# Optimization experiments

Hardware: AMD Instinct MI355X
Metric: run time of the kernel (lower is better)

## Reference

```python
import jax, jax.numpy as jnp
import numpy as np

T_STEPS = 200
B = 512
D = 32
LMBD = 1.0


def _socm_const_m_loss(ts, states, noises, controls, nabla_V, nabla_f,
                       nabla_b, nabla_g, sigma, log_pd, log_ps, log_tw):
    # ts: [T+1]; states/nabla_V: [T+1,B,D]; noises/controls/nabla_f: [T,B,D];
    # nabla_b: [T,B,D,D]; nabla_g: [B,D]; sigma: [D,D]; logs: [B]
    sigma_inv_T = jnp.linalg.inv(sigma).T

    # integrand terms on the first T timesteps ([:-1] slice in torch source)
    term1 = nabla_f  # nabla_f(ts[0], states)[:-1]
    sig_noises = jnp.einsum('ij,abj->abi', sigma_inv_T, noises)
    term2 = -np.sqrt(LMBD) * jnp.einsum('abij,abj->abi', nabla_b, sig_noises)
    sig_controls = jnp.einsum('ij,abj->abi', sigma_inv_T, controls)
    term3 = -jnp.einsum('abij,abj->abi', nabla_b, sig_controls)

    dts = ts[1:] - ts[:-1]                      # [T]
    dts_ = dts[:, None, None]
    zeros = jnp.zeros_like(term1[:1])           # [1,B,D]

    t1_dt = jnp.concatenate([zeros, term1 * dts_], axis=0)             # [T+1,B,D]
    t2_sdt = jnp.concatenate([zeros, term2 * jnp.sqrt(dts_)], axis=0)
    t3_dt = jnp.concatenate([zeros, term3 * dts_], axis=0)

    def rev_cum(x):
        # total_sum - cumsum == reverse cumulative sum starting at each step
        return jnp.sum(x, axis=0, keepdims=True) - jnp.cumsum(x, axis=0)

    least_squares_target = (rev_cum(t1_dt) + rev_cum(t2_sdt) + rev_cum(t3_dt)
                            + nabla_g[None, :, :])                     # [T+1,B,D]

    control_learned = -jnp.einsum('ij,tbj->tbi', sigma.T, nabla_V)
    control_target = -jnp.einsum('ij,tbj->tbi', sigma.T, least_squares_target)

    weight = jnp.exp(log_pd + log_ps + log_tw)  # [B]
    sq = (control_learned - control_target) ** 2 * weight[None, :, None]
    n_t, n_b = states.shape[0], states.shape[1]
    return jnp.sum(sq) / (n_t * n_b)


def setup_inputs() -> dict:
    key = jax.random.key(0)
    ks = jax.random.split(key, 11)
    ts = jnp.linspace(0.0, 1.0, T_STEPS + 1, dtype=jnp.float32)
    states = jax.random.normal(ks[0], (T_STEPS + 1, B, D), jnp.float32)
    noises = jax.random.normal(ks[1], (T_STEPS, B, D), jnp.float32)
    controls = jax.random.normal(ks[2], (T_STEPS, B, D), jnp.float32)
    nabla_V = jax.random.normal(ks[3], (T_STEPS + 1, B, D), jnp.float32)
    nabla_f = jax.random.normal(ks[4], (T_STEPS, B, D), jnp.float32)
    nabla_b = 0.1 * jax.random.normal(ks[5], (T_STEPS, B, D, D), jnp.float32)
    nabla_g = jax.random.normal(ks[6], (B, D), jnp.float32)
    sigma = jnp.eye(D, dtype=jnp.float32) + 0.05 * jax.random.normal(ks[7], (D, D), jnp.float32)
    log_pd = 0.01 * jax.random.normal(ks[8], (B,), jnp.float32)
    log_ps = 0.01 * jax.random.normal(ks[9], (B,), jnp.float32)
    log_tw = 0.01 * jax.random.normal(ks[10], (B,), jnp.float32)
    return {"ts": ts, "states": states, "noises": noises, "controls": controls,
            "nabla_V": nabla_V, "nabla_f": nabla_f, "nabla_b": nabla_b,
            "nabla_g": nabla_g, "sigma": sigma, "log_pd": log_pd,
            "log_ps": log_ps, "log_tw": log_tw}


def reference(ts, states, noises, controls, nabla_V, nabla_f, nabla_b,
              nabla_g, sigma, log_pd, log_ps, log_tw):
    return _socm_const_m_loss(ts, states, noises, controls, nabla_V, nabla_f,
                              nabla_b, nabla_g, sigma, log_pd, log_ps, log_tw)
```

## Files before the change

### kernel.cpp

```cpp
#include <hip/hip_runtime.h>
#include <math.h>

#define T_STEPS 200
#define BB 512
#define DD 32
#define LMBD 1.0f
#define NCH 4
#define CHT 50

#define WS_MINV 0
#define WS_A    1024
#define WS_W    2048
#define WS_PART 2560
#define WS_CT   3072
#define WS_Y    (3072 + 65536)
#define WS_M    (3072 + 131072)

__global__ __launch_bounds__(512) void prep_kernel(
    const float* __restrict__ sigma,
    const float* __restrict__ lpd, const float* __restrict__ lps,
    const float* __restrict__ ltw,
    float* __restrict__ ws)
{
    __shared__ float sg[32][33];
    const int tid = threadIdx.x;

    ws[WS_W + tid] = expf(lpd[tid] + lps[tid] + ltw[tid]);

    for (int idx = tid; idx < 1024; idx += 512)
        sg[idx >> 5][idx & 31] = sigma[idx];
    __syncthreads();

    for (int idx = tid; idx < 1024; idx += 512) {
        int i = idx >> 5, j = idx & 31;
        float s = 0.0f;
        #pragma unroll
        for (int k = 0; k < 32; ++k) s += sg[i][k] * sg[j][k];
        ws[WS_A + idx] = s;
    }

    if (tid < 64) {
        const int l = tid;
        float col[32];
        #pragma unroll
        for (int r = 0; r < 32; ++r) {
            float v = sg[r][l & 31];
            col[r] = (l < 32) ? v : ((r == (l - 32)) ? 1.0f : 0.0f);
        }
        #pragma unroll
        for (int k = 0; k < 32; ++k) {
            float pinv = 1.0f / __shfl(col[k], k);
            col[k] *= pinv;
            #pragma unroll
            for (int r = 0; r < 32; ++r) {
                if (r == k) continue;
                float f = __shfl(col[r], k);
                col[r] -= f * col[k];
            }
        }
        if (l >= 32) {
            #pragma unroll
            for (int r = 0; r < 32; ++r)
                ws[WS_MINV + (l - 32) * 32 + r] = col[r];
        }
    }
}

__global__ __launch_bounds__(256) void stream_kernel(
    const float* __restrict__ ts,
    const float* __restrict__ noises,
    const float* __restrict__ controls,
    const float* __restrict__ nabla_f,
    const float* __restrict__ nabla_V,
    const float* __restrict__ nabla_b,
    float* __restrict__ ws)
{
    __shared__ float ts_l[52];
    __shared__ __align__(16) float buf[2][4][32];
    __shared__ __align__(16) float vls[32];
    __shared__ __align__(16) float yls[32];
    __shared__ float red[256];

    const int h   = blockIdx.x;
    const int b   = blockIdx.y;
    const int tid = threadIdx.x;
    const int r   = tid >> 3;
    const int q   = tid & 7;
    const int w   = tid >> 6;
    const int lane = tid & 63;

    const int t0 = h * CHT, t1 = t0 + CHT;

    const float* sp_w = (w == 0) ? noises : (w == 1) ? controls
                       : (w == 2) ? nabla_f : nabla_V;

    if (tid < 51) ts_l[tid] = ts[t0 + tid];
    if (lane < 32) buf[0][w][lane] = sp_w[((size_t)t0 * BB + b) * DD + lane];

    float4 Minv4 = *(const float4*)(ws + WS_MINV + r * 32 + 4 * q);
    float4 nbCur = ((const float4*)nabla_b + (size_t)(t0 * BB + b) * 256)[tid];

    float P = 0.0f, Yacc = 0.0f;
    float a0 = 0.f, a1 = 0.f, a2 = 0.f, a3 = 0.f;
    __syncthreads();

    for (int t = t0; t < t1; ++t) {
        const int p = t & 1;
        const int tn = (t + 1 < t1) ? t + 1 : t1 - 1;
        float4 nbNext = ((const float4*)nabla_b + (size_t)(tn * BB + b) * 256)[tid];
        float smallNext = 0.0f;
        if (lane < 32) smallNext = sp_w[((size_t)tn * BB + b) * DD + lane];

        const float dt  = ts_l[t - t0 + 1] - ts_l[t - t0];
        const float sdt = sqrtf(LMBD * dt);

        {
            float4 n4 = *(const float4*)&buf[p][0][4 * q];
            float4 c4 = *(const float4*)&buf[p][1][4 * q];
            float wx = -sdt * n4.x - dt * c4.x;
            float wy = -sdt * n4.y - dt * c4.y;
            float wz = -sdt * n4.z - dt * c4.z;
            float ww = -sdt * n4.w - dt * c4.w;
            float pv = Minv4.x * wx + Minv4.y * wy + Minv4.z * wz + Minv4.w * ww;
            pv += __shfl_xor(pv, 1);
            pv += __shfl_xor(pv, 2);
            pv += __shfl_xor(pv, 4);
            if (q == 0) vls[r] = pv;
        }
        __syncthreads();

        float yr;
        {
            float Vt = buf[p][3][r];
            yr = P + Vt;
            if (q == 0) yls[r] = yr;
            float4 v4 = *(const float4*)&vls[4 * q];
            float pc = nbCur.x * v4.x + nbCur.y * v4.y
                     + nbCur.z * v4.z + nbCur.w * v4.w;
            pc += __shfl_xor(pc, 1);
            pc += __shfl_xor(pc, 2);
            pc += __shfl_xor(pc, 4);
            float fr = buf[p][2][r];
            P += dt * fr + pc;
            Yacc += yr;
        }
        __syncthreads();

        {
            float4 y4 = *(const float4*)&yls[4 * q];
            a0 += yr * y4.x; a1 += yr * y4.y; a2 += yr * y4.z; a3 += yr * y4.w;
        }
        if (lane < 32) buf[p ^ 1][w][lane] = smallNext;
        nbCur = nbNext;
        __syncthreads();
    }

    if (h == NCH - 1) {
        float Vt = nabla_V[((size_t)T_STEPS * BB + b) * DD + r];
        float yr = P + Vt;
        if (q == 0) yls[r] = yr;
        Yacc += yr;
        __syncthreads();
        float4 y4 = *(const float4*)&yls[4 * q];
        a0 += yr * y4.x; a1 += yr * y4.y; a2 += yr * y4.z; a3 += yr * y4.w;
        __syncthreads();
    }

    {
        float4 A4 = *(const float4*)(ws + WS_A + r * 32 + 4 * q);
        float mp = a0 * A4.x + a1 * A4.y + a2 * A4.z + a3 * A4.w;
        red[tid] = mp;
        __syncthreads();
        for (int st = 128; st > 0; st >>= 1) {
            if (tid < st) red[tid] += red[tid + st];
            __syncthreads();
        }
        if (q == 0) {
            ws[WS_CT + (b * NCH + h) * 32 + r] = P;
            ws[WS_Y  + (b * NCH + h) * 32 + r] = Yacc;
        }
        if (tid == 0) ws[WS_M + b * NCH + h] = red[0];
    }
}

__global__ __launch_bounds__(256) void combine_kernel(
    const float* __restrict__ nabla_g,
    float* __restrict__ ws)
{
    __shared__ float ct[NCH][32], Yl[NCH][32];
    __shared__ float Sv[32], Cp[32];
    __shared__ __align__(16) float sp[32];
    __shared__ float red[32];

    const int b   = blockIdx.x;
    const int tid = threadIdx.x;
    const int r   = tid >> 3;
    const int q   = tid & 7;

    if (tid < NCH * 32) {
        int hh = tid >> 5, i = tid & 31;
        ct[hh][i] = ws[WS_CT + (b * NCH + hh) * 32 + i];
        Yl[hh][i] = ws[WS_Y  + (b * NCH + hh) * 32 + i];
    }
    if (tid < 32) Cp[tid] = 0.0f;
    __syncthreads();
    if (tid < 32) {
        float s = nabla_g[b * 32 + tid];
        #pragma unroll
        for (int hh = 0; hh < NCH; ++hh) s += ct[hh][tid];
        Sv[tid] = s;
    }

    float acc = 0.0f;
    float4 A4 = *(const float4*)(ws + WS_A + r * 32 + 4 * q);
    for (int hh = 0; hh < NCH; ++hh) {
        __syncthreads();
        if (tid < 32) sp[tid] = Sv[tid] - Cp[tid];
        __syncthreads();
        float4 s4 = *(const float4*)&sp[4 * q];
        float as = A4.x * s4.x + A4.y * s4.y + A4.z * s4.z + A4.w * s4.w;
        as += __shfl_xor(as, 1);
        as += __shfl_xor(as, 2);
        as += __shfl_xor(as, 4);
        float nh = (hh == NCH - 1) ? (float)(CHT + 1) : (float)CHT;
        if (q == 0) acc += as * (nh * sp[r] - 2.0f * Yl[hh][r]);
        if (tid < 32) Cp[tid] += ct[hh][tid];
    }
    __syncthreads();
    if (q == 0) red[r] = acc;
    __syncthreads();
    if (tid == 0) {
        float s = 0.0f;
        #pragma unroll
        for (int i = 0; i < 32; ++i) s += red[i];
        #pragma unroll
        for (int hh = 0; hh < NCH; ++hh) s += ws[WS_M + b * NCH + hh];
        ws[WS_PART + b] = ws[WS_W + b] * s;
    }
}

__global__ __launch_bounds__(512) void reduce_kernel(
    const float* __restrict__ ws, float* __restrict__ out)
{
    __shared__ float r[512];
    const int tid = threadIdx.x;
    r[tid] = ws[WS_PART + tid];
    __syncthreads();
    for (int st = 256; st > 0; st >>= 1) {
        if (tid < st) r[tid] += r[tid + st];
        __syncthreads();
    }
    if (tid == 0) out[0] = r[0] * (1.0f / (201.0f * 512.0f));
}

extern "C" void kernel_launch(void* const* d_in, const int* in_sizes, int n_in,
                              void* d_out, int out_size, void* d_ws, size_t ws_size,
                              hipStream_t stream) {
    (void)in_sizes; (void)n_in; (void)out_size; (void)ws_size;
    const float* ts       = (const float*)d_in[0];
    const float* noises   = (const float*)d_in[2];
    const float* controls = (const float*)d_in[3];
    const float* nabla_V  = (const float*)d_in[4];
    const float* nabla_f  = (const float*)d_in[5];
    const float* nabla_b  = (const float*)d_in[6];
    const float* nabla_g  = (const float*)d_in[7];
    const float* sigma    = (const float*)d_in[8];
    const float* lpd      = (const float*)d_in[9];
    const float* lps      = (const float*)d_in[10];
    const float* ltw      = (const float*)d_in[11];
    float* ws  = (float*)d_ws;
    float* out = (float*)d_out;

    prep_kernel<<<1, 512, 0, stream>>>(sigma, lpd, lps, ltw, ws);
    stream_kernel<<<dim3(NCH, BB), 256, 0, stream>>>(ts, noises, controls,
                                                     nabla_f, nabla_V, nabla_b, ws);
    combine_kernel<<<BB, 256, 0, stream>>>(nabla_g, ws);
    reduce_kernel<<<1, 512, 0, stream>>>(ws, out);
}
```

Measured before the change: 111.1 us.

## Rewrite stream kernel as single-wavefront shuffle pipeline with more time chunks

The stream kernel now runs one 64-lane wavefront per (chunk, batch) block and does all exchanges with register shuffles instead of shared memory. This removes the three block-wide barriers per timestep and the shared-memory tree reduction. The time axis is split into twice as many chunks, giving more blocks in flight to hide the serial dependence on the running prefix. dt and sqrt(dt) are now precomputed in the prep kernel. The trade-off is that each lane holds more nabla_b registers per step and issues many more shuffles, and the combine kernel has more partial chunks to merge.

```diff
diff --git a/kernel.cpp b/kernel.cpp
--- a/kernel.cpp
+++ b/kernel.cpp
@@ -5,18 +5,21 @@
 #define BB 512
 #define DD 32
 #define LMBD 1.0f
-#define NCH 4
-#define CHT 50
+#define NCH 8
+#define CHT 25
 
 #define WS_MINV 0
 #define WS_A    1024
 #define WS_W    2048
 #define WS_PART 2560
-#define WS_CT   3072
-#define WS_Y    (3072 + 65536)
-#define WS_M    (3072 + 131072)
+#define WS_DT   3072
+#define WS_SDT  3328
+#define WS_CT   4096
+#define WS_Y    135168
+#define WS_M    266240
 
 __global__ __launch_bounds__(512) void prep_kernel(
+    const float* __restrict__ ts,
     const float* __restrict__ sigma,
     const float* __restrict__ lpd, const float* __restrict__ lps,
     const float* __restrict__ ltw,
@@ -26,6 +29,13 @@
     const int tid = threadIdx.x;
 
     ws[WS_W + tid] = expf(lpd[tid] + lps[tid] + ltw[tid]);
+
+    if (tid < T_STEPS) {
+        float a = ts[tid], b = ts[tid + 1];
+        float dt = b - a;
+        ws[WS_DT + tid]  = dt;
+        ws[WS_SDT + tid] = sqrtf(LMBD * dt);
+    }
 
     for (int idx = tid; idx < 1024; idx += 512)
         sg[idx >> 5][idx & 31] = sigma[idx];
@@ -66,8 +76,7 @@
     }
 }
 
-__global__ __launch_bounds__(256) void stream_kernel(
-    const float* __restrict__ ts,
+__global__ __launch_bounds__(64) void stream_kernel(
     const float* __restrict__ noises,
     const float* __restrict__ controls,
     const float* __restrict__ nabla_f,
@@ -75,112 +84,150 @@
     const float* __restrict__ nabla_b,
     float* __restrict__ ws)
 {
-    __shared__ float ts_l[52];
-    __shared__ __align__(16) float buf[2][4][32];
-    __shared__ __align__(16) float vls[32];
-    __shared__ __align__(16) float yls[32];
-    __shared__ float red[256];
-
-    const int h   = blockIdx.x;
-    const int b   = blockIdx.y;
-    const int tid = threadIdx.x;
-    const int r   = tid >> 3;
-    const int q   = tid & 7;
-    const int w   = tid >> 6;
-    const int lane = tid & 63;
+    const int h = blockIdx.x;
+    const int b = blockIdx.y;
+    const int l = threadIdx.x;
+    const int j = l & 31;
+    const int half = l >> 5;
+    const int cg = l & 7;
+    const int rg = l >> 3;
 
     const int t0 = h * CHT, t1 = t0 + CHT;
 
-    const float* sp_w = (w == 0) ? noises : (w == 1) ? controls
-                       : (w == 2) ? nabla_f : nabla_V;
-
-    if (tid < 51) ts_l[tid] = ts[t0 + tid];
-    if (lane < 32) buf[0][w][lane] = sp_w[((size_t)t0 * BB + b) * DD + lane];
-
-    float4 Minv4 = *(const float4*)(ws + WS_MINV + r * 32 + 4 * q);
-    float4 nbCur = ((const float4*)nabla_b + (size_t)(t0 * BB + b) * 256)[tid];
+    float Mv[16];
+    #pragma unroll
+    for (int c = 0; c < 16; ++c)
+        Mv[c] = ws[WS_MINV + j * 32 + 16 * half + c];
+
+    const float* sm1p = (half == 0) ? noises  : controls;
+    const float* sm2p = (half == 0) ? nabla_f : nabla_V;
+
+    const float4* nb = (const float4*)nabla_b;
+
+    size_t tf4 = (size_t)(t0 * BB + b) * 256;
+    float4 n0 = nb[tf4 + l];
+    float4 n1 = nb[tf4 + l + 64];
+    float4 n2 = nb[tf4 + l + 128];
+    float4 n3 = nb[tf4 + l + 192];
+    float s1 = sm1p[(size_t)(t0 * BB + b) * DD + j];
+    float s2 = sm2p[(size_t)(t0 * BB + b) * DD + j];
 
     float P = 0.0f, Yacc = 0.0f;
-    float a0 = 0.f, a1 = 0.f, a2 = 0.f, a3 = 0.f;
-    __syncthreads();
+    float M00=0,M01=0,M02=0,M03=0, M10=0,M11=0,M12=0,M13=0;
+    float M20=0,M21=0,M22=0,M23=0, M30=0,M31=0,M32=0,M33=0;
 
     for (int t = t0; t < t1; ++t) {
-        const int p = t & 1;
-        const int tn = (t + 1 < t1) ? t + 1 : t1 - 1;
-        float4 nbNext = ((const float4*)nabla_b + (size_t)(tn * BB + b) * 256)[tid];
-        float smallNext = 0.0f;
-        if (lane < 32) smallNext = sp_w[((size_t)tn * BB + b) * DD + lane];
-
-        const float dt  = ts_l[t - t0 + 1] - ts_l[t - t0];
-        const float sdt = sqrtf(LMBD * dt);
-
-        {
-            float4 n4 = *(const float4*)&buf[p][0][4 * q];
-            float4 c4 = *(const float4*)&buf[p][1][4 * q];
-            float wx = -sdt * n4.x - dt * c4.x;
-            float wy = -sdt * n4.y - dt * c4.y;
-            float wz = -sdt * n4.z - dt * c4.z;
-            float ww = -sdt * n4.w - dt * c4.w;
-            float pv = Minv4.x * wx + Minv4.y * wy + Minv4.z * wz + Minv4.w * ww;
-            pv += __shfl_xor(pv, 1);
-            pv += __shfl_xor(pv, 2);
-            pv += __shfl_xor(pv, 4);
-            if (q == 0) vls[r] = pv;
-        }
-        __syncthreads();
-
-        float yr;
-        {
-            float Vt = buf[p][3][r];
-            yr = P + Vt;
-            if (q == 0) yls[r] = yr;
-            float4 v4 = *(const float4*)&vls[4 * q];
-            float pc = nbCur.x * v4.x + nbCur.y * v4.y
-                     + nbCur.z * v4.z + nbCur.w * v4.w;
-            pc += __shfl_xor(pc, 1);
-            pc += __shfl_xor(pc, 2);
-            pc += __shfl_xor(pc, 4);
-            float fr = buf[p][2][r];
-            P += dt * fr + pc;
-            Yacc += yr;
-        }
-        __syncthreads();
-
-        {
-            float4 y4 = *(const float4*)&yls[4 * q];
-            a0 += yr * y4.x; a1 += yr * y4.y; a2 += yr * y4.z; a3 += yr * y4.w;
-        }
-        if (lane < 32) buf[p ^ 1][w][lane] = smallNext;
-        nbCur = nbNext;
-        __syncthreads();
+        const int tn = (t + 1 < t1) ? t + 1 : t;
+        size_t tf4n = (size_t)(tn * BB + b) * 256;
+        float4 m0 = nb[tf4n + l];
+        float4 m1 = nb[tf4n + l + 64];
+        float4 m2 = nb[tf4n + l + 128];
+        float4 m3 = nb[tf4n + l + 192];
+        float s1n = sm1p[(size_t)(tn * BB + b) * DD + j];
+        float s2n = sm2p[(size_t)(tn * BB + b) * DD + j];
+
+        const float dt  = ws[WS_DT + t];
+        const float sdt = ws[WS_SDT + t];
+
+        float o1 = __shfl_xor(s1, 32);
+        float o2 = __shfl_xor(s2, 32);
+        float nse = (half == 0) ? s1 : o1;
+        float ctl = (half == 0) ? o1 : s1;
+        float fv  = (half == 0) ? s2 : o2;
+        float Vv  = (half == 0) ? o2 : s2;
+
+        float w = -sdt * nse - dt * ctl;
+
+        float part = 0.0f;
+        #pragma unroll
+        for (int c = 0; c < 16; ++c)
+            part += Mv[c] * __shfl(w, 16 * half + c);
+        float v = part + __shfl_xor(part, 32);
+
+        float y = P + Vv;
+        Yacc += y;
+
+        float vg0 = __shfl(v, 4 * cg + 0);
+        float vg1 = __shfl(v, 4 * cg + 1);
+        float vg2 = __shfl(v, 4 * cg + 2);
+        float vg3 = __shfl(v, 4 * cg + 3);
+        float d0 = n0.x*vg0 + n0.y*vg1 + n0.z*vg2 + n0.w*vg3;
+        float d1 = n1.x*vg0 + n1.y*vg1 + n1.z*vg2 + n1.w*vg3;
+        float d2 = n2.x*vg0 + n2.y*vg1 + n2.z*vg2 + n2.w*vg3;
+        float d3 = n3.x*vg0 + n3.y*vg1 + n3.z*vg2 + n3.w*vg3;
+        d0 += __shfl_xor(d0,1); d0 += __shfl_xor(d0,2); d0 += __shfl_xor(d0,4);
+        d1 += __shfl_xor(d1,1); d1 += __shfl_xor(d1,2); d1 += __shfl_xor(d1,4);
+        d2 += __shfl_xor(d2,1); d2 += __shfl_xor(d2,2); d2 += __shfl_xor(d2,4);
+        d3 += __shfl_xor(d3,1); d3 += __shfl_xor(d3,2); d3 += __shfl_xor(d3,4);
+        float g0 = __shfl(d0, 8 * (l & 7));
+        float g1 = __shfl(d1, 8 * (l & 7));
+        float g2 = __shfl(d2, 8 * (l & 7));
+        float g3 = __shfl(d3, 8 * (l & 7));
+        const int slot = (l >> 3) & 3;
+        float pA = (slot & 1) ? g1 : g0;
+        float pB = (slot & 1) ? g3 : g2;
+        float pc = (slot & 2) ? pB : pA;
+
+        P += dt * fv + pc;
+
+        float yr0 = __shfl(y, rg + 0);
+        float yr1 = __shfl(y, rg + 8);
+        float yr2 = __shfl(y, rg + 16);
+        float yr3 = __shfl(y, rg + 24);
+        float yc0 = __shfl(y, 4 * cg + 0);
+        float yc1 = __shfl(y, 4 * cg + 1);
+        float yc2 = __shfl(y, 4 * cg + 2);
+        float yc3 = __shfl(y, 4 * cg + 3);
+        M00 += yr0*yc0; M01 += yr0*yc1; M02 += yr0*yc2; M03 += yr0*yc3;
+        M10 += yr1*yc0; M11 += yr1*yc1; M12 += yr1*yc2; M13 += yr1*yc3;
+        M20 += yr2*yc0; M21 += yr2*yc1; M22 += yr2*yc2; M23 += yr2*yc3;
+        M30 += yr3*yc0; M31 += yr3*yc1; M32 += yr3*yc2; M33 += yr3*yc3;
+
+        n0 = m0; n1 = m1; n2 = m2; n3 = m3; s1 = s1n; s2 = s2n;
     }
 
     if (h == NCH - 1) {
-        float Vt = nabla_V[((size_t)T_STEPS * BB + b) * DD + r];
-        float yr = P + Vt;
-        if (q == 0) yls[r] = yr;
-        Yacc += yr;
-        __syncthreads();
-        float4 y4 = *(const float4*)&yls[4 * q];
-        a0 += yr * y4.x; a1 += yr * y4.y; a2 += yr * y4.z; a3 += yr * y4.w;
-        __syncthreads();
-    }
-
+        float Vt = nabla_V[((size_t)T_STEPS * BB + b) * DD + j];
+        float y = P + Vt;
+        Yacc += y;
+        float yr0 = __shfl(y, rg + 0);
+        float yr1 = __shfl(y, rg + 8);
+        float yr2 = __shfl(y, rg + 16);
+        float yr3 = __shfl(y, rg + 24);
+        float yc0 = __shfl(y, 4 * cg + 0);
+        float yc1 = __shfl(y, 4 * cg + 1);
+        float yc2 = __shfl(y, 4 * cg + 2);
+        float yc3 = __shfl(y, 4 * cg + 3);
+        M00 += yr0*yc0; M01 += yr0*yc1; M02 += yr0*yc2; M03 += yr0*yc3;
+        M10 += yr1*yc0; M11 += yr1*yc1; M12 += yr1*yc2; M13 += yr1*yc3;
+        M20 += yr2*yc0; M21 += yr2*yc1; M22 += yr2*yc2; M23 += yr2*yc3;
+        M30 += yr3*yc0; M31 += yr3*yc1; M32 += yr3*yc2; M33 += yr3*yc3;
+    }
+
+    float mpart = 0.0f;
     {
-        float4 A4 = *(const float4*)(ws + WS_A + r * 32 + 4 * q);
-        float mp = a0 * A4.x + a1 * A4.y + a2 * A4.z + a3 * A4.w;
-        red[tid] = mp;
-        __syncthreads();
-        for (int st = 128; st > 0; st >>= 1) {
-            if (tid < st) red[tid] += red[tid + st];
-            __syncthreads();
-        }
-        if (q == 0) {
-            ws[WS_CT + (b * NCH + h) * 32 + r] = P;
-            ws[WS_Y  + (b * NCH + h) * 32 + r] = Yacc;
-        }
-        if (tid == 0) ws[WS_M + b * NCH + h] = red[0];
-    }
+        const float* Ab = ws + WS_A;
+        float4 A0 = *(const float4*)(Ab + (rg +  0) * 32 + 4 * cg);
+        float4 A1 = *(const float4*)(Ab + (rg +  8) * 32 + 4 * cg);
+        float4 A2 = *(const float4*)(Ab + (rg + 16) * 32 + 4 * cg);
+        float4 A3 = *(const float4*)(Ab + (rg + 24) * 32 + 4 * cg);
+        mpart = M00*A0.x + M01*A0.y + M02*A0.z + M03*A0.w
+              + M10*A1.x + M11*A1.y + M12*A1.z + M13*A1.w
+              + M20*A2.x + M21*A2.y + M22*A2.z + M23*A2.w
+              + M30*A3.x + M31*A3.y + M32*A3.z + M33*A3.w;
+    }
+    mpart += __shfl_xor(mpart, 1);
+    mpart += __shfl_xor(mpart, 2);
+    mpart += __shfl_xor(mpart, 4);
+    mpart += __shfl_xor(mpart, 8);
+    mpart += __shfl_xor(mpart, 16);
+    mpart += __shfl_xor(mpart, 32);
+
+    if (half == 0) {
+        ws[WS_CT + (b * NCH + h) * 32 + j] = P;
+        ws[WS_Y  + (b * NCH + h) * 32 + j] = Yacc;
+    }
+    if (l == 0) ws[WS_M + b * NCH + h] = mpart;
 }
 
 __global__ __launch_bounds__(256) void combine_kernel(
@@ -197,7 +244,7 @@
     const int r   = tid >> 3;
     const int q   = tid & 7;
 
-    if (tid < NCH * 32) {
+    {
         int hh = tid >> 5, i = tid & 31;
         ct[hh][i] = ws[WS_CT + (b * NCH + hh) * 32 + i];
         Yl[hh][i] = ws[WS_Y  + (b * NCH + hh) * 32 + i];
@@ -271,9 +318,9 @@
     float* ws  = (float*)d_ws;
     float* out = (float*)d_out;
 
-    prep_kernel<<<1, 512, 0, stream>>>(sigma, lpd, lps, ltw, ws);
-    stream_kernel<<<dim3(NCH, BB), 256, 0, stream>>>(ts, noises, controls,
-                                                     nabla_f, nabla_V, nabla_b, ws);
+    prep_kernel<<<1, 512, 0, stream>>>(ts, sigma, lpd, lps, ltw, ws);
+    stream_kernel<<<dim3(NCH, BB), 64, 0, stream>>>(noises, controls, nabla_f,
+                                                    nabla_V, nabla_b, ws);
     combine_kernel<<<BB, 256, 0, stream>>>(nabla_g, ws);
     reduce_kernel<<<1, 512, 0, stream>>>(ws, out);
 }
```

Result: slower. 115.2 us (+3.6%).

## Precompute sigma-inverse noise/control products in a separate kernel, cut stream barriers

Applied to the files above, without the earlier changes.

Moves the Minv·(−sdt·noise − dt·control) product out of the sequential time loop into a new fully parallel v_kernel that writes per-step vectors to workspace. dt and sqrt(dt) are also precomputed in prep_kernel. The stream kernel now loads the precomputed vector directly and goes from three barriers per step to one, using double-buffered y storage. The cost is an extra kernel launch plus a write and read of about 13 MB of intermediate data in workspace.

```diff
diff --git a/kernel.cpp b/kernel.cpp
--- a/kernel.cpp
+++ b/kernel.cpp
@@ -12,11 +12,15 @@
 #define WS_A    1024
 #define WS_W    2048
 #define WS_PART 2560
-#define WS_CT   3072
-#define WS_Y    (3072 + 65536)
-#define WS_M    (3072 + 131072)
+#define WS_DT   3072
+#define WS_SDT  3328
+#define WS_V    4096
+#define WS_CT   3280896
+#define WS_Y    3346432
+#define WS_M    3411968
 
 __global__ __launch_bounds__(512) void prep_kernel(
+    const float* __restrict__ ts,
     const float* __restrict__ sigma,
     const float* __restrict__ lpd, const float* __restrict__ lps,
     const float* __restrict__ ltw,
@@ -26,6 +30,13 @@
     const int tid = threadIdx.x;
 
     ws[WS_W + tid] = expf(lpd[tid] + lps[tid] + ltw[tid]);
+
+    if (tid < T_STEPS) {
+        float a = ts[tid], b = ts[tid + 1];
+        float dt = b - a;
+        ws[WS_DT + tid]  = dt;
+        ws[WS_SDT + tid] = sqrtf(LMBD * dt);
+    }
 
     for (int idx = tid; idx < 1024; idx += 512)
         sg[idx >> 5][idx & 31] = sigma[idx];
@@ -66,19 +77,51 @@
     }
 }
 
-__global__ __launch_bounds__(256) void stream_kernel(
-    const float* __restrict__ ts,
+__global__ __launch_bounds__(256) void v_kernel(
     const float* __restrict__ noises,
     const float* __restrict__ controls,
+    float* __restrict__ ws)
+{
+    __shared__ __align__(16) float wsm[8][36];
+    const int tid = threadIdx.x;
+    const int uu = tid >> 5, j = tid & 31;
+    const int unit = blockIdx.x * 8 + uu;
+    const int t = unit >> 9;
+
+    const float dt  = ws[WS_DT + t];
+    const float sdt = ws[WS_SDT + t];
+
+    const size_t g = (size_t)unit * DD + j;
+    float nv = noises[g], cv = controls[g];
+    wsm[uu][j] = -sdt * nv - dt * cv;
+
+    float4 mr[8];
+    {
+        const float4* mp = (const float4*)(ws + WS_MINV + j * 32);
+        #pragma unroll
+        for (int c = 0; c < 8; ++c) mr[c] = mp[c];
+    }
+    __syncthreads();
+
+    float v = 0.0f;
+    {
+        const float4* wr = (const float4*)wsm[uu];
+        #pragma unroll
+        for (int c = 0; c < 8; ++c) {
+            float4 a = wr[c];
+            v += mr[c].x * a.x + mr[c].y * a.y + mr[c].z * a.z + mr[c].w * a.w;
+        }
+    }
+    ws[WS_V + g] = v;
+}
+
+__global__ __launch_bounds__(256) void stream_kernel(
     const float* __restrict__ nabla_f,
     const float* __restrict__ nabla_V,
     const float* __restrict__ nabla_b,
     float* __restrict__ ws)
 {
-    __shared__ float ts_l[52];
-    __shared__ __align__(16) float buf[2][4][32];
-    __shared__ __align__(16) float vls[32];
-    __shared__ __align__(16) float yls[32];
+    __shared__ __align__(16) float yls[2][32];
     __shared__ float red[256];
 
     const int h   = blockIdx.x;
@@ -86,101 +129,72 @@
     const int tid = threadIdx.x;
     const int r   = tid >> 3;
     const int q   = tid & 7;
-    const int w   = tid >> 6;
-    const int lane = tid & 63;
 
     const int t0 = h * CHT, t1 = t0 + CHT;
-
-    const float* sp_w = (w == 0) ? noises : (w == 1) ? controls
-                       : (w == 2) ? nabla_f : nabla_V;
-
-    if (tid < 51) ts_l[tid] = ts[t0 + tid];
-    if (lane < 32) buf[0][w][lane] = sp_w[((size_t)t0 * BB + b) * DD + lane];
-
-    float4 Minv4 = *(const float4*)(ws + WS_MINV + r * 32 + 4 * q);
-    float4 nbCur = ((const float4*)nabla_b + (size_t)(t0 * BB + b) * 256)[tid];
+    const float4* nb = (const float4*)nabla_b;
+
+    int base = (t0 * BB + b) * DD;
+    float4 nbC = nb[(size_t)base * 8 + tid];
+    float4 v4C = *(const float4*)(ws + WS_V + base + 4 * q);
+    float  fC  = nabla_f[base + r];
+    float  VC  = nabla_V[base + r];
 
     float P = 0.0f, Yacc = 0.0f;
     float a0 = 0.f, a1 = 0.f, a2 = 0.f, a3 = 0.f;
-    __syncthreads();
 
     for (int t = t0; t < t1; ++t) {
+        const int tn = (t + 1 < t1) ? t + 1 : t;
+        const int basen = (tn * BB + b) * DD;
+        float4 nbN = nb[(size_t)basen * 8 + tid];
+        float4 v4N = *(const float4*)(ws + WS_V + basen + 4 * q);
+        float  fN  = nabla_f[basen + r];
+        float  VN  = nabla_V[basen + r];
+
+        const float dt = ws[WS_DT + t];
         const int p = t & 1;
-        const int tn = (t + 1 < t1) ? t + 1 : t1 - 1;
-        float4 nbNext = ((const float4*)nabla_b + (size_t)(tn * BB + b) * 256)[tid];
-        float smallNext = 0.0f;
-        if (lane < 32) smallNext = sp_w[((size_t)tn * BB + b) * DD + lane];
-
-        const float dt  = ts_l[t - t0 + 1] - ts_l[t - t0];
-        const float sdt = sqrtf(LMBD * dt);
-
-        {
-            float4 n4 = *(const float4*)&buf[p][0][4 * q];
-            float4 c4 = *(const float4*)&buf[p][1][4 * q];
-            float wx = -sdt * n4.x - dt * c4.x;
-            float wy = -sdt * n4.y - dt * c4.y;
-            float wz = -sdt * n4.z - dt * c4.z;
-            float ww = -sdt * n4.w - dt * c4.w;
-            float pv = Minv4.x * wx + Minv4.y * wy + Minv4.z * wz + Minv4.w * ww;
-            pv += __shfl_xor(pv, 1);
-            pv += __shfl_xor(pv, 2);
-            pv += __shfl_xor(pv, 4);
-            if (q == 0) vls[r] = pv;
-        }
-        __syncthreads();
-
-        float yr;
-        {
-            float Vt = buf[p][3][r];
-            yr = P + Vt;
-            if (q == 0) yls[r] = yr;
-            float4 v4 = *(const float4*)&vls[4 * q];
-            float pc = nbCur.x * v4.x + nbCur.y * v4.y
-                     + nbCur.z * v4.z + nbCur.w * v4.w;
-            pc += __shfl_xor(pc, 1);
-            pc += __shfl_xor(pc, 2);
-            pc += __shfl_xor(pc, 4);
-            float fr = buf[p][2][r];
-            P += dt * fr + pc;
-            Yacc += yr;
-        }
-        __syncthreads();
-
-        {
-            float4 y4 = *(const float4*)&yls[4 * q];
-            a0 += yr * y4.x; a1 += yr * y4.y; a2 += yr * y4.z; a3 += yr * y4.w;
-        }
-        if (lane < 32) buf[p ^ 1][w][lane] = smallNext;
-        nbCur = nbNext;
-        __syncthreads();
+
+        float y = P + VC;
+        Yacc += y;
+        if (q == 0) yls[p][r] = y;
+
+        float pc = nbC.x * v4C.x + nbC.y * v4C.y + nbC.z * v4C.z + nbC.w * v4C.w;
+        pc += __shfl_xor(pc, 1);
+        pc += __shfl_xor(pc, 2);
+        pc += __shfl_xor(pc, 4);
+        P += dt * fC + pc;
+
+        __syncthreads();
+
+        float4 y4 = *(const float4*)&yls[p][4 * q];
+        a0 += y * y4.x; a1 += y * y4.y; a2 += y * y4.z; a3 += y * y4.w;
+
+        nbC = nbN; v4C = v4N; fC = fN; VC = VN;
     }
 
     if (h == NCH - 1) {
         float Vt = nabla_V[((size_t)T_STEPS * BB + b) * DD + r];
-        float yr = P + Vt;
-        if (q == 0) yls[r] = yr;
-        Yacc += yr;
-        __syncthreads();
-        float4 y4 = *(const float4*)&yls[4 * q];
-        a0 += yr * y4.x; a1 += yr * y4.y; a2 += yr * y4.z; a3 += yr * y4.w;
-        __syncthreads();
-    }
-
-    {
-        float4 A4 = *(const float4*)(ws + WS_A + r * 32 + 4 * q);
-        float mp = a0 * A4.x + a1 * A4.y + a2 * A4.z + a3 * A4.w;
-        red[tid] = mp;
-        __syncthreads();
-        for (int st = 128; st > 0; st >>= 1) {
-            if (tid < st) red[tid] += red[tid + st];
-            __syncthreads();
-        }
-        if (q == 0) {
-            ws[WS_CT + (b * NCH + h) * 32 + r] = P;
-            ws[WS_Y  + (b * NCH + h) * 32 + r] = Yacc;
-        }
-        if (tid == 0) ws[WS_M + b * NCH + h] = red[0];
-    }
+        float y = P + Vt;
+        Yacc += y;
+        if (q == 0) yls[0][r] = y;
+        __syncthreads();
+        float4 y4 = *(const float4*)&yls[0][4 * q];
+        a0 += y * y4.x; a1 += y * y4.y; a2 += y * y4.z; a3 += y * y4.w;
+    }
+
+    float4 A4 = *(const float4*)(ws + WS_A + r * 32 + 4 * q);
+    float mpart = a0 * A4.x + a1 * A4.y + a2 * A4.z + a3 * A4.w;
+    __syncthreads();
+    red[tid] = mpart;
+    __syncthreads();
+    for (int st = 128; st > 0; st >>= 1) {
+        if (tid < st) red[tid] += red[tid + st];
+        __syncthreads();
+    }
+    if (q == 0) {
+        ws[WS_CT + (b * NCH + h) * 32 + r] = P;
+        ws[WS_Y  + (b * NCH + h) * 32 + r] = Yacc;
+    }
+    if (tid == 0) ws[WS_M + b * NCH + h] = red[0];
 }
 
 __global__ __launch_bounds__(256) void combine_kernel(
@@ -271,9 +285,10 @@
     float* ws  = (float*)d_ws;
     float* out = (float*)d_out;
 
-    prep_kernel<<<1, 512, 0, stream>>>(sigma, lpd, lps, ltw, ws);
-    stream_kernel<<<dim3(NCH, BB), 256, 0, stream>>>(ts, noises, controls,
-                                                     nabla_f, nabla_V, nabla_b, ws);
+    prep_kernel<<<1, 512, 0, stream>>>(ts, sigma, lpd, lps, ltw, ws);
+    v_kernel<<<(T_STEPS * BB) / 8, 256, 0, stream>>>(noises, controls, ws);
+    stream_kernel<<<dim3(NCH, BB), 256, 0, stream>>>(nabla_f, nabla_V,
+                                                     nabla_b, ws);
     combine_kernel<<<BB, 256, 0, stream>>>(nabla_g, ws);
     reduce_kernel<<<1, 512, 0, stream>>>(ws, out);
 }
```

Result: slower. 156.9 us (+41.2%).
